# Optimization experiments

Measured on AMD Instinct MI355X. Metric: run time of the kernel, lower is better.

## Reference

```python
import jax, jax.numpy as jnp
import numpy as np

SEQ_LEN = 70      # hardcoded in original (view(-1, 70))
HIDDEN = 230
EMB = 50
VOCAB = 100000
BIG_NUM = 64
N_TOTAL = 2048
N_REL = 100       # hardcoded relation count
POS_VOCAB = 123
POS_DIM = 5
D_IN = EMB + 2 * POS_DIM


def setup_inputs() -> dict:
    key = jax.random.key(0)
    ks = jax.random.split(key, 20)
    bag = N_TOTAL // BIG_NUM
    labels = jax.random.randint(ks[3], (BIG_NUM,), 0, N_REL)
    inp = {
        "sentence": jax.random.randint(ks[0], (N_TOTAL, SEQ_LEN), 0, VOCAB),
        "pos1": jax.random.randint(ks[1], (N_TOTAL, SEQ_LEN), 0, POS_VOCAB),
        "pos2": jax.random.randint(ks[2], (N_TOTAL, SEQ_LEN), 0, POS_VOCAB),
        "total_shape": jnp.arange(BIG_NUM + 1, dtype=jnp.int32) * bag,
        "y_batch": jax.nn.one_hot(labels, N_REL, dtype=jnp.float32),
        "word_emb": jax.random.normal(ks[4], (VOCAB, EMB), jnp.float32) * 0.1,
        "pos1_table": jax.random.normal(ks[5], (POS_VOCAB, POS_DIM), jnp.float32) * 0.1,
        "pos2_table": jax.random.normal(ks[6], (POS_VOCAB, POS_DIM), jnp.float32) * 0.1,
        "W_ih_f": jax.random.normal(ks[7], (3 * HIDDEN, D_IN), jnp.float32) * 0.05,
        "W_hh_f": jax.random.normal(ks[8], (3 * HIDDEN, HIDDEN), jnp.float32) * 0.05,
        "b_ih_f": jnp.zeros((3 * HIDDEN,), jnp.float32),
        "b_hh_f": jnp.zeros((3 * HIDDEN,), jnp.float32),
        "W_ih_b": jax.random.normal(ks[9], (3 * HIDDEN, D_IN), jnp.float32) * 0.05,
        "W_hh_b": jax.random.normal(ks[10], (3 * HIDDEN, HIDDEN), jnp.float32) * 0.05,
        "b_ih_b": jnp.zeros((3 * HIDDEN,), jnp.float32),
        "b_hh_b": jnp.zeros((3 * HIDDEN,), jnp.float32),
        "attention_w": jax.random.normal(ks[11], (HIDDEN, 1), jnp.float32) * 0.1,
        "sen_a": jax.random.normal(ks[12], (HIDDEN,), jnp.float32) * 0.1,
        "sen_r": jax.random.normal(ks[13], (HIDDEN, 1), jnp.float32) * 0.1,
        "relation_embedding": jax.random.normal(ks[14], (N_REL, HIDDEN), jnp.float32) * 0.1,
        "sen_d": jax.random.normal(ks[15], (N_REL,), jnp.float32) * 0.1,
    }
    return inp


def _gru_dir(x_proj, W_hh, b_hh, reverse):
    """One GRU direction. x_proj: [N,T,3H] = x @ W_ih^T + b_ih (precomputed)."""
    N = x_proj.shape[0]
    H = W_hh.shape[1]

    def step(h, gi):
        gh = h @ W_hh.T + b_hh
        i_r, i_z, i_n = jnp.split(gi, 3, axis=-1)
        h_r, h_z, h_n = jnp.split(gh, 3, axis=-1)
        r = jax.nn.sigmoid(i_r + h_r)
        z = jax.nn.sigmoid(i_z + h_z)
        n = jnp.tanh(i_n + r * h_n)
        h = (1.0 - z) * n + z * h
        return h, h

    h0 = jnp.zeros((N, H), x_proj.dtype)
    _, ys = jax.lax.scan(step, h0, jnp.swapaxes(x_proj, 0, 1), reverse=reverse)
    return jnp.swapaxes(ys, 0, 1)  # [N,T,H]


def reference(sentence, pos1, pos2, total_shape, y_batch,
              word_emb, pos1_table, pos2_table,
              W_ih_f, W_hh_f, b_ih_f, b_hh_f,
              W_ih_b, W_hh_b, b_ih_b, b_hh_b,
              attention_w, sen_a, sen_r, relation_embedding, sen_d):
    # embedding lookup + concat -> [N, T, D_IN]
    emb = jnp.concatenate([word_emb[sentence], pos1_table[pos1], pos2_table[pos2]], axis=-1)
    gi_f = jnp.einsum('ntd,gd->ntg', emb, W_ih_f) + b_ih_f
    gi_b = jnp.einsum('ntd,gd->ntg', emb, W_ih_b) + b_ih_b
    # bidirectional GRU, then sum fwd + bwd halves (torch.add(tupf, tupb))
    tup = _gru_dir(gi_f, W_hh_f, b_hh_f, False) + _gru_dir(gi_b, W_hh_b, b_hh_b, True)  # [N,T,H]
    # word-level attention over the 70 timesteps
    word_alpha = jax.nn.softmax((jnp.tanh(tup) @ attention_w)[..., 0], axis=-1)  # [N,T]
    attention_r = jnp.einsum('nt,nth->nh', word_alpha, tup)                       # [N,H]
    repre = jnp.tanh(attention_r)
    # ragged per-bag (sentence-level) attention via segment ops
    n_total = repre.shape[0]
    seg = jnp.searchsorted(total_shape[1:], jnp.arange(n_total), side='right')   # [N] bag ids
    s = ((repre * sen_a) @ sen_r)[:, 0]                                          # [N]
    m = jax.ops.segment_max(s, seg, num_segments=BIG_NUM)
    e = jnp.exp(s - m[seg])
    denom = jax.ops.segment_sum(e, seg, num_segments=BIG_NUM)
    alpha = e / denom[seg]
    sen_s = jax.ops.segment_sum(alpha[:, None] * repre, seg, num_segments=BIG_NUM)  # [B,H]
    logits = sen_s @ relation_embedding.T + sen_d                                   # [B,100]
    prob = jax.nn.softmax(logits, axis=-1)
    # BCEWithLogitsLoss (mean over 100 classes) summed over bags
    bce = jnp.maximum(logits, 0.0) - logits * y_batch + jnp.log1p(jnp.exp(-jnp.abs(logits)))
    total_loss = jnp.sum(jnp.mean(bce, axis=-1))
    acc = (jnp.argmax(prob, axis=-1) == jnp.argmax(y_batch, axis=-1)).astype(jnp.float32)
    return total_loss, acc, prob
```

## Files before the change

kernel.cpp:

```cpp
#include <hip/hip_runtime.h>
#include <hip/hip_bf16.h>
#include <math.h>

#define SEQ 70
#define HID 230
#define G3  690
#define EMBD 50
#define DIN 60
#define NTOT 2048
#define NREL 100
#define NBAG 64
#define BAGSZ 32
#define PDIM 5
#define MB 8


__global__ void k_zero(float* p, long n) {
    long i = (long)blockIdx.x * 256 + threadIdx.x;
    if (i < n) p[i] = 0.f;
}

__global__ void k_embed(const int* __restrict__ sent, const int* __restrict__ p1,
                        const int* __restrict__ p2,  const float* __restrict__ wemb,
                        const float* __restrict__ t1, const float* __restrict__ t2,
                        float* __restrict__ emb) {
    long idx = (long)blockIdx.x * 256 + threadIdx.x;
    long total = (long)NTOT * SEQ * DIN;
    if (idx >= total) return;
    int nt = (int)(idx / DIN);
    int j  = (int)(idx % DIN);
    float v;
    if (j < EMBD)            v = wemb[(long)sent[nt] * EMBD + j];
    else if (j < EMBD + PDIM) v = t1[p1[nt] * PDIM + (j - EMBD)];
    else                      v = t2[p2[nt] * PDIM + (j - EMBD - PDIM)];
    emb[idx] = v;
}

__global__ void k_transpose(const float* __restrict__ in, float* __restrict__ out,
                            int G, int K) {
    int idx = blockIdx.x * 256 + threadIdx.x;
    if (idx >= G * K) return;
    int g = idx / K, k = idx % K;
    out[k * G + g] = in[idx];
}

__global__ __launch_bounds__(256) void k_gru(
    const float* __restrict__ emb,
    const float* __restrict__ wihT_f, const float* __restrict__ whhT_f,
    const float* __restrict__ bih_f,  const float* __restrict__ bhh_f,
    const float* __restrict__ wihT_b, const float* __restrict__ whhT_b,
    const float* __restrict__ bih_b,  const float* __restrict__ bhh_b,
    float* __restrict__ tup) {

    const bool rev = blockIdx.x & 1;
    const int  n0  = (blockIdx.x >> 1) * MB;
    const float* wihT = rev ? wihT_b : wihT_f;
    const float* whhT = rev ? whhT_b : whhT_f;
    const float* bih  = rev ? bih_b  : bih_f;
    const float* bhh  = rev ? bhh_b  : bhh_f;
    const int tid = threadIdx.x;

    __shared__ float h_s[HID * MB];
    __shared__ float e_s[DIN * MB];
    __shared__ float P_s[G3 * MB];
    __shared__ float Q_s[HID * MB];

    for (int i = tid; i < HID * MB; i += 256) h_s[i] = 0.f;

    const int g0 = tid;
    const int g1 = tid + 256;
    const int g2 = tid + 512;
    const bool v2 = (g2 < G3);

    const float bi0 = bih[g0], bh0 = bhh[g0];
    const float bi1 = bih[g1], bh1 = bhh[g1];
    const float bi2 = v2 ? bih[g2] : 0.f, bh2 = v2 ? bhh[g2] : 0.f;

    for (int t = 0; t < SEQ; ++t) {
        const int tt = rev ? (SEQ - 1 - t) : t;

        for (int i = tid; i < DIN * MB; i += 256) {
            int n = i / DIN, k = i - n * DIN;
            e_s[k * MB + n] = emb[((long)(n0 + n) * SEQ + tt) * DIN + k];
        }
        __syncthreads();

        float a0[MB], a1[MB], a2[MB], h0[MB], h1[MB], h2[MB];
#pragma unroll
        for (int n = 0; n < MB; ++n) {
            a0[n] = bi0; a1[n] = bi1; a2[n] = bi2;
            h0[n] = bh0; h1[n] = bh1; h2[n] = bh2;
        }
        for (int k = 0; k < DIN; ++k) {
            float w0 = wihT[k * G3 + g0];
            float w1 = wihT[k * G3 + g1];
            float w2 = v2 ? wihT[k * G3 + g2] : 0.f;
            const float4* ep = (const float4*)&e_s[k * MB];
            float4 ea = ep[0], eb = ep[1];
            float ev[8] = {ea.x, ea.y, ea.z, ea.w, eb.x, eb.y, eb.z, eb.w};
#pragma unroll
            for (int n = 0; n < MB; ++n) {
                a0[n] = fmaf(w0, ev[n], a0[n]);
                a1[n] = fmaf(w1, ev[n], a1[n]);
                a2[n] = fmaf(w2, ev[n], a2[n]);
            }
        }
        for (int k = 0; k < HID; ++k) {
            float w0 = whhT[k * G3 + g0];
            float w1 = whhT[k * G3 + g1];
            float w2 = v2 ? whhT[k * G3 + g2] : 0.f;
            const float4* hp = (const float4*)&h_s[k * MB];
            float4 ha = hp[0], hb = hp[1];
            float hv[8] = {ha.x, ha.y, ha.z, ha.w, hb.x, hb.y, hb.z, hb.w};
#pragma unroll
            for (int n = 0; n < MB; ++n) {
                h0[n] = fmaf(w0, hv[n], h0[n]);
                h1[n] = fmaf(w1, hv[n], h1[n]);
                h2[n] = fmaf(w2, hv[n], h2[n]);
            }
        }
#pragma unroll
        for (int n = 0; n < MB; ++n) P_s[g0 * MB + n] = a0[n] + h0[n];
        if (g1 < 2 * HID) {
#pragma unroll
            for (int n = 0; n < MB; ++n) P_s[g1 * MB + n] = a1[n] + h1[n];
        } else {
#pragma unroll
            for (int n = 0; n < MB; ++n) {
                P_s[g1 * MB + n] = a1[n];
                Q_s[(g1 - 2 * HID) * MB + n] = h1[n];
            }
        }
        if (v2) {
#pragma unroll
            for (int n = 0; n < MB; ++n) {
                P_s[g2 * MB + n] = a2[n];
                Q_s[(g2 - 2 * HID) * MB + n] = h2[n];
            }
        }
        __syncthreads();

        for (int e = tid; e < HID * MB; e += 256) {
            int n = e / HID, hh = e - n * HID;
            int idx = hh * MB + n;
            float r = 1.f / (1.f + expf(-P_s[idx]));
            float z = 1.f / (1.f + expf(-P_s[(HID + hh) * MB + n]));
            float nn = tanhf(P_s[(2 * HID + hh) * MB + n] + r * Q_s[idx]);
            float hold = h_s[idx];
            float hnew = (1.f - z) * nn + z * hold;
            h_s[idx] = hnew;
            atomicAdd(&tup[((long)(n0 + n) * SEQ + tt) * HID + hh], hnew);
        }
    }
}

__global__ __launch_bounds__(256) void k_wordattn(
    const float* __restrict__ tup, const float* __restrict__ attw,
    const float* __restrict__ sen_a, const float* __restrict__ sen_r,
    float* __restrict__ repre, float* __restrict__ sbuf) {
    const int n = blockIdx.x, tid = threadIdx.x;
    __shared__ float tl[SEQ * HID];
    __shared__ float sc[SEQ];
    __shared__ float red[4];
    for (int i = tid; i < SEQ * HID; i += 256) tl[i] = tup[(long)n * SEQ * HID + i];
    __syncthreads();
    if (tid < SEQ) {
        float s = 0.f;
        for (int h = 0; h < HID; ++h) s += tanhf(tl[tid * HID + h]) * attw[h];
        sc[tid] = s;
    }
    __syncthreads();
    if (tid == 0) {
        float m = sc[0];
        for (int t = 1; t < SEQ; ++t) m = fmaxf(m, sc[t]);
        float ssum = 0.f;
        for (int t = 0; t < SEQ; ++t) { float e = expf(sc[t] - m); sc[t] = e; ssum += e; }
        float inv = 1.f / ssum;
        for (int t = 0; t < SEQ; ++t) sc[t] *= inv;
    }
    __syncthreads();
    float part = 0.f;
    if (tid < HID) {
        float r = 0.f;
        for (int t = 0; t < SEQ; ++t) r = fmaf(sc[t], tl[t * HID + tid], r);
        float rep = tanhf(r);
        repre[(long)n * HID + tid] = rep;
        part = rep * sen_a[tid] * sen_r[tid];
    }
    for (int off = 32; off; off >>= 1) part += __shfl_down(part, off, 64);
    if ((tid & 63) == 0) red[tid >> 6] = part;
    __syncthreads();
    if (tid == 0) sbuf[n] = red[0] + red[1] + red[2] + red[3];
}

__global__ __launch_bounds__(256) void k_bag(
    const float* __restrict__ repre, const float* __restrict__ sbuf,
    const float* __restrict__ rel, const float* __restrict__ sen_d,
    const float* __restrict__ y, float* __restrict__ out, float* __restrict__ bagloss) {
    const int b = blockIdx.x, tid = threadIdx.x;
    __shared__ float al[BAGSZ];
    __shared__ float ss[HID];
    __shared__ float lg[NREL];
    if (tid == 0) {
        float m = -1e30f;
        for (int i = 0; i < BAGSZ; ++i) m = fmaxf(m, sbuf[b * BAGSZ + i]);
        float s = 0.f;
        for (int i = 0; i < BAGSZ; ++i) { float e = expf(sbuf[b * BAGSZ + i] - m); al[i] = e; s += e; }
        float inv = 1.f / s;
        for (int i = 0; i < BAGSZ; ++i) al[i] *= inv;
    }
    __syncthreads();
    if (tid < HID) {
        float acc = 0.f;
        for (int i = 0; i < BAGSZ; ++i)
            acc = fmaf(al[i], repre[(long)(b * BAGSZ + i) * HID + tid], acc);
        ss[tid] = acc;
    }
    __syncthreads();
    if (tid < NREL) {
        float acc = sen_d[tid];
        for (int h = 0; h < HID; ++h) acc = fmaf(ss[h], rel[tid * HID + h], acc);
        lg[tid] = acc;
    }
    __syncthreads();
    if (tid == 0) {
        float m = -1e30f; int am = 0;
        for (int r = 0; r < NREL; ++r) if (lg[r] > m) { m = lg[r]; am = r; }
        float s = 0.f;
        for (int r = 0; r < NREL; ++r) s += expf(lg[r] - m);
        float inv = 1.f / s;
        float ym = -1e30f; int ay = 0;
        for (int r = 0; r < NREL; ++r) { float yy = y[b * NREL + r]; if (yy > ym) { ym = yy; ay = r; } }
        out[1 + b] = (am == ay) ? 1.f : 0.f;
        float loss = 0.f;
        for (int r = 0; r < NREL; ++r) {
            float l = lg[r], yy = y[b * NREL + r];
            loss += fmaxf(l, 0.f) - l * yy + log1pf(expf(-fabsf(l)));
            out[1 + NBAG + b * NREL + r] = expf(l - m) * inv;
        }
        bagloss[b] = loss / NREL;
    }
}

__global__ void k_final(const float* __restrict__ bagloss, float* __restrict__ out) {
    if (blockIdx.x == 0 && threadIdx.x == 0) {
        float s = 0.f;
        for (int i = 0; i < NBAG; ++i) s += bagloss[i];
        out[0] = s;
    }
}

extern "C" void kernel_launch(void* const* d_in, const int* in_sizes, int n_in,
                              void* d_out, int out_size, void* d_ws, size_t ws_size,
                              hipStream_t stream) {
    const int*   sent   = (const int*)d_in[0];
    const int*   pos1   = (const int*)d_in[1];
    const int*   pos2   = (const int*)d_in[2];
    const float* ybatch = (const float*)d_in[4];
    const float* wemb   = (const float*)d_in[5];
    const float* p1tab  = (const float*)d_in[6];
    const float* p2tab  = (const float*)d_in[7];
    const float* Wih_f  = (const float*)d_in[8];
    const float* Whh_f  = (const float*)d_in[9];
    const float* bih_f  = (const float*)d_in[10];
    const float* bhh_f  = (const float*)d_in[11];
    const float* Wih_b  = (const float*)d_in[12];
    const float* Whh_b  = (const float*)d_in[13];
    const float* bih_b  = (const float*)d_in[14];
    const float* bhh_b  = (const float*)d_in[15];
    const float* attw   = (const float*)d_in[16];
    const float* sen_a  = (const float*)d_in[17];
    const float* sen_r  = (const float*)d_in[18];
    const float* rel    = (const float*)d_in[19];
    const float* sen_d  = (const float*)d_in[20];
    float* out = (float*)d_out;

    float* ws = (float*)d_ws;
    size_t off = 0;
    float* emb    = ws + off; off += (size_t)NTOT * SEQ * DIN;
    float* wihT_f = ws + off; off += (size_t)DIN * G3;
    float* wihT_b = ws + off; off += (size_t)DIN * G3;
    float* whhT_f = ws + off; off += (size_t)HID * G3;
    float* whhT_b = ws + off; off += (size_t)HID * G3;
    float* tup    = ws + off; off += (size_t)NTOT * SEQ * HID;
    float* repre  = ws + off; off += (size_t)NTOT * HID;
    float* sbuf   = ws + off; off += (size_t)NTOT;
    float* bagloss= ws + off; off += (size_t)NBAG;

    const long tupN = (long)NTOT * SEQ * HID;
    k_zero<<<(int)((tupN + 255) / 256), 256, 0, stream>>>(tup, tupN);

    const long embN = (long)NTOT * SEQ * DIN;
    k_embed<<<(int)((embN + 255) / 256), 256, 0, stream>>>(sent, pos1, pos2, wemb, p1tab, p2tab, emb);

    k_transpose<<<(G3 * DIN + 255) / 256, 256, 0, stream>>>(Wih_f, wihT_f, G3, DIN);
    k_transpose<<<(G3 * DIN + 255) / 256, 256, 0, stream>>>(Wih_b, wihT_b, G3, DIN);
    k_transpose<<<(G3 * HID + 255) / 256, 256, 0, stream>>>(Whh_f, whhT_f, G3, HID);
    k_transpose<<<(G3 * HID + 255) / 256, 256, 0, stream>>>(Whh_b, whhT_b, G3, HID);

    k_gru<<<(NTOT / MB) * 2, 256, 0, stream>>>(emb,
        wihT_f, whhT_f, bih_f, bhh_f,
        wihT_b, whhT_b, bih_b, bhh_b, tup);

    k_wordattn<<<NTOT, 256, 0, stream>>>(tup, attw, sen_a, sen_r, repre, sbuf);

    k_bag<<<NBAG, 256, 0, stream>>>(repre, sbuf, rel, sen_d, ybatch, out, bagloss);

    k_final<<<1, 64, 0, stream>>>(bagloss, out);
}
```

Before: 2.918 ms.

## Restructure GRU so each thread owns one hidden unit's three gates over 16 sequences

The GRU kernel now assigns each of 230 active threads one hidden unit and computes its r, z and n gate pre-activations in registers, so the gate nonlinearity and state update happen in-thread. This removes the P_s/Q_s shared staging buffers and one round of shared-memory traffic per timestep. The per-block sentence batch doubles from 8 to 16, which halves the number of blocks and doubles weight reuse per load. In exchange, 26 of 256 threads sit idle, register pressure roughly doubles (96 accumulators), and only 256 blocks are launched, which may underfill the GPU.

```diff
diff --git a/kernel.cpp b/kernel.cpp
--- a/kernel.cpp
+++ b/kernel.cpp
@@ -12,7 +12,7 @@
 #define NBAG 64
 #define BAGSZ 32
 #define PDIM 5
-#define MB 8
+#define MB 16
 
 
 __global__ void k_zero(float* p, long n) {
@@ -59,97 +59,89 @@
     const float* bih  = rev ? bih_b  : bih_f;
     const float* bhh  = rev ? bhh_b  : bhh_f;
     const int tid = threadIdx.x;
-
-    __shared__ float h_s[HID * MB];
-    __shared__ float e_s[DIN * MB];
-    __shared__ float P_s[G3 * MB];
-    __shared__ float Q_s[HID * MB];
-
-    for (int i = tid; i < HID * MB; i += 256) h_s[i] = 0.f;
-
-    const int g0 = tid;
-    const int g1 = tid + 256;
-    const int g2 = tid + 512;
-    const bool v2 = (g2 < G3);
-
-    const float bi0 = bih[g0], bh0 = bhh[g0];
-    const float bi1 = bih[g1], bh1 = bhh[g1];
-    const float bi2 = v2 ? bih[g2] : 0.f, bh2 = v2 ? bhh[g2] : 0.f;
+    const bool act = tid < HID;
+
+    __shared__ float h_s[HID][MB];
+    __shared__ float e_s[DIN][MB];
+
+    for (int i = tid; i < HID * MB; i += 256) ((float*)h_s)[i] = 0.f;
+
+    float bir = 0.f, biz = 0.f, bin_ = 0.f, bhr = 0.f, bhz = 0.f, bhn = 0.f;
+    if (act) {
+        bir = bih[tid]; biz = bih[HID + tid]; bin_ = bih[2 * HID + tid];
+        bhr = bhh[tid]; bhz = bhh[HID + tid]; bhn = bhh[2 * HID + tid];
+    }
+    float hprev[MB];
+#pragma unroll
+    for (int n = 0; n < MB; ++n) hprev[n] = 0.f;
+
+    const float* wi = wihT + tid;
+    const float* wh = whhT + tid;
+
+    __syncthreads();
 
     for (int t = 0; t < SEQ; ++t) {
         const int tt = rev ? (SEQ - 1 - t) : t;
 
         for (int i = tid; i < DIN * MB; i += 256) {
             int n = i / DIN, k = i - n * DIN;
-            e_s[k * MB + n] = emb[((long)(n0 + n) * SEQ + tt) * DIN + k];
+            e_s[k][n] = emb[((long)(n0 + n) * SEQ + tt) * DIN + k];
         }
         __syncthreads();
 
-        float a0[MB], a1[MB], a2[MB], h0[MB], h1[MB], h2[MB];
-#pragma unroll
-        for (int n = 0; n < MB; ++n) {
-            a0[n] = bi0; a1[n] = bi1; a2[n] = bi2;
-            h0[n] = bh0; h1[n] = bh1; h2[n] = bh2;
-        }
-        for (int k = 0; k < DIN; ++k) {
-            float w0 = wihT[k * G3 + g0];
-            float w1 = wihT[k * G3 + g1];
-            float w2 = v2 ? wihT[k * G3 + g2] : 0.f;
-            const float4* ep = (const float4*)&e_s[k * MB];
-            float4 ea = ep[0], eb = ep[1];
-            float ev[8] = {ea.x, ea.y, ea.z, ea.w, eb.x, eb.y, eb.z, eb.w};
+        float ar[MB], az[MB], an[MB], hr[MB], hz[MB], hn[MB];
+        if (act) {
 #pragma unroll
             for (int n = 0; n < MB; ++n) {
-                a0[n] = fmaf(w0, ev[n], a0[n]);
-                a1[n] = fmaf(w1, ev[n], a1[n]);
-                a2[n] = fmaf(w2, ev[n], a2[n]);
+                ar[n] = bir; az[n] = biz; an[n] = bin_;
+                hr[n] = bhr; hz[n] = bhz; hn[n] = bhn;
             }
-        }
-        for (int k = 0; k < HID; ++k) {
-            float w0 = whhT[k * G3 + g0];
-            float w1 = whhT[k * G3 + g1];
-            float w2 = v2 ? whhT[k * G3 + g2] : 0.f;
-            const float4* hp = (const float4*)&h_s[k * MB];
-            float4 ha = hp[0], hb = hp[1];
-            float hv[8] = {ha.x, ha.y, ha.z, ha.w, hb.x, hb.y, hb.z, hb.w};
-#pragma unroll
-            for (int n = 0; n < MB; ++n) {
-                h0[n] = fmaf(w0, hv[n], h0[n]);
-                h1[n] = fmaf(w1, hv[n], h1[n]);
-                h2[n] = fmaf(w2, hv[n], h2[n]);
+#pragma unroll 4
+            for (int k = 0; k < DIN; ++k) {
+                float wr = wi[k * G3];
+                float wz = wi[k * G3 + HID];
+                float wn = wi[k * G3 + 2 * HID];
+                const float4* ep = (const float4*)e_s[k];
+                float4 e0 = ep[0], e1 = ep[1], e2 = ep[2], e3 = ep[3];
+                float ev[MB] = {e0.x, e0.y, e0.z, e0.w, e1.x, e1.y, e1.z, e1.w,
+                                e2.x, e2.y, e2.z, e2.w, e3.x, e3.y, e3.z, e3.w};
+#pragma unroll
+                for (int n = 0; n < MB; ++n) {
+                    ar[n] = fmaf(wr, ev[n], ar[n]);
+                    az[n] = fmaf(wz, ev[n], az[n]);
+                    an[n] = fmaf(wn, ev[n], an[n]);
+                }
             }
-        }
-#pragma unroll
-        for (int n = 0; n < MB; ++n) P_s[g0 * MB + n] = a0[n] + h0[n];
-        if (g1 < 2 * HID) {
-#pragma unroll
-            for (int n = 0; n < MB; ++n) P_s[g1 * MB + n] = a1[n] + h1[n];
-        } else {
-#pragma unroll
-            for (int n = 0; n < MB; ++n) {
-                P_s[g1 * MB + n] = a1[n];
-                Q_s[(g1 - 2 * HID) * MB + n] = h1[n];
-            }
-        }
-        if (v2) {
-#pragma unroll
-            for (int n = 0; n < MB; ++n) {
-                P_s[g2 * MB + n] = a2[n];
-                Q_s[(g2 - 2 * HID) * MB + n] = h2[n];
+#pragma unroll 2
+            for (int k = 0; k < HID; ++k) {
+                float wr = wh[k * G3];
+                float wz = wh[k * G3 + HID];
+                float wn = wh[k * G3 + 2 * HID];
+                const float4* hp = (const float4*)h_s[k];
+                float4 h0 = hp[0], h1 = hp[1], h2 = hp[2], h3 = hp[3];
+                float hv[MB] = {h0.x, h0.y, h0.z, h0.w, h1.x, h1.y, h1.z, h1.w,
+                                h2.x, h2.y, h2.z, h2.w, h3.x, h3.y, h3.z, h3.w};
+#pragma unroll
+                for (int n = 0; n < MB; ++n) {
+                    hr[n] = fmaf(wr, hv[n], hr[n]);
+                    hz[n] = fmaf(wz, hv[n], hz[n]);
+                    hn[n] = fmaf(wn, hv[n], hn[n]);
+                }
             }
         }
         __syncthreads();
 
-        for (int e = tid; e < HID * MB; e += 256) {
-            int n = e / HID, hh = e - n * HID;
-            int idx = hh * MB + n;
-            float r = 1.f / (1.f + expf(-P_s[idx]));
-            float z = 1.f / (1.f + expf(-P_s[(HID + hh) * MB + n]));
-            float nn = tanhf(P_s[(2 * HID + hh) * MB + n] + r * Q_s[idx]);
-            float hold = h_s[idx];
-            float hnew = (1.f - z) * nn + z * hold;
-            h_s[idx] = hnew;
-            atomicAdd(&tup[((long)(n0 + n) * SEQ + tt) * HID + hh], hnew);
+        if (act) {
+#pragma unroll
+            for (int n = 0; n < MB; ++n) {
+                float r  = 1.f / (1.f + expf(-(ar[n] + hr[n])));
+                float z  = 1.f / (1.f + expf(-(az[n] + hz[n])));
+                float nn = tanhf(an[n] + r * hn[n]);
+                float hnew = (1.f - z) * nn + z * hprev[n];
+                hprev[n] = hnew;
+                h_s[tid][n] = hnew;
+                atomicAdd(&tup[((long)(n0 + n) * SEQ + tt) * HID + tid], hnew);
+            }
         }
     }
 }
```

New measurement: 3.518 ms. 20.6% more time.
